# Kernel tuning notes

Measured on AMD Instinct MI355X. Metric: run time of the kernel, lower is better.

Reference implementation:

```python
import jax, jax.numpy as jnp
import numpy as np

B, C, H, W = 4, 128, 256, 256
N, NPOS, KS = 4000, 8, 3
CH = 2 * NPOS  # mask=False -> 2*n_pos offset channels


def setup_inputs() -> dict:
    key = jax.random.key(0)
    ks = jax.random.split(key, 8)
    x = jax.random.normal(ks[0], (B, C, H, W), jnp.float32)
    keypoints = jax.random.uniform(ks[1], (B, N, 2), jnp.float32) * 2.0 - 1.0  # [-1,1]
    w1 = jax.random.normal(ks[2], (CH, C, KS, KS), jnp.float32) * 0.05  # offset conv 3x3
    b1 = jnp.zeros((CH,), jnp.float32)
    w2 = jax.random.normal(ks[3], (CH, CH), jnp.float32) * 0.05        # offset conv 1x1
    b2 = jnp.zeros((CH,), jnp.float32)
    wsf = jax.random.normal(ks[4], (C, C), jnp.float32) * 0.05         # sf_conv 1x1 no bias
    agg_weights = jax.random.uniform(ks[5], (NPOS, C, C), jnp.float32)  # torch.rand init
    return {"x": x, "keypoints": keypoints, "w1": w1, "b1": b1, "w2": w2,
            "b2": b2, "wsf": wsf, "agg_weights": agg_weights}


def _bilinear_sample(img, px, py):
    """grid_sample(mode=bilinear, align_corners=True, padding=zeros) at pixel coords.
    img: (C,H,W); px,py: (M,). Returns (C,M)."""
    c, h, w = img.shape
    x0f = jnp.floor(px); y0f = jnp.floor(py)
    x0 = x0f.astype(jnp.int32); y0 = y0f.astype(jnp.int32)
    wx1 = px - x0f; wx0 = 1.0 - wx1
    wy1 = py - y0f; wy0 = 1.0 - wy1

    def tap(xi, yi, wgt):
        valid = ((xi >= 0) & (xi < w) & (yi >= 0) & (yi < h)).astype(img.dtype)
        v = img[:, jnp.clip(yi, 0, h - 1), jnp.clip(xi, 0, w - 1)]  # (C,M)
        return v * (wgt * valid)

    return (tap(x0, y0, wx0 * wy0) + tap(x0 + 1, y0, wx1 * wy0)
            + tap(x0, y0 + 1, wx0 * wy1) + tap(x0 + 1, y0 + 1, wx1 * wy1))


def _per_image(xi, kpts, w1, b1, w2, b2, wsf, agg_weights):
    wh = jnp.array([W - 1.0, H - 1.0], xi.dtype)
    max_offset = max(H, W) / 4.0
    kwh = (kpts / 2.0 + 0.5) * wh                      # (N,2) pixel coords, >=0
    rc = kwh.astype(jnp.int32)                          # .long() trunc (positive)
    corner = jnp.trunc(rc.astype(jnp.float32) - KS / 2.0 + 1.0).astype(jnp.int32)
    cx = jnp.clip(corner[:, 0], 0, W - 1 - KS)
    cy = jnp.clip(corner[:, 1], 0, H - 1 - KS)
    ar = jnp.arange(KS)
    # patch[n,c,a,b] = xi[c, cy_n+a, cx_n+b]
    patch = xi[:, (cy[:, None] + ar)[:, :, None], (cx[:, None] + ar)[:, None, :]]  # (C,N,KS,KS)
    patch = patch.transpose(1, 0, 2, 3)                 # (N,C,KS,KS)
    # offset network: 3x3 conv (valid) on 3x3 patch == full contraction, then ReLU, 1x1 conv
    h1 = jax.nn.relu(jnp.einsum('nchw,ochw->no', patch, w1) + b1)
    off = jnp.clip(h1 @ w2.T + b2, -max_offset, max_offset)  # (N, 2*NPOS)
    off = off.reshape(-1, 2, NPOS).transpose(0, 2, 1)        # (N,NPOS,2)
    # deform sampling positions; torch normalizes then grid_sample(align_corners=True)
    # maps exactly back to pixel coords, so sample at pixel coords directly
    pos = kwh[:, None, :] + off                              # (N,NPOS,2)
    feats = _bilinear_sample(xi, pos[..., 0].reshape(-1), pos[..., 1].reshape(-1))  # (C,N*NPOS)
    feats = feats.reshape(C, -1, NPOS).transpose(1, 0, 2)    # (N,C,NPOS)
    feats = jax.nn.selu(jnp.einsum('ncp,dc->ndp', feats, wsf))
    descs = jnp.einsum('ncp,pcd->nd', feats, agg_weights)    # (N,C)
    descs = descs / jnp.maximum(jnp.linalg.norm(descs, axis=1, keepdims=True), 1e-12)
    return descs, off


def reference(x, keypoints, w1, b1, w2, b2, wsf, agg_weights):
    f = jax.vmap(lambda xi, k: _per_image(xi, k, w1, b1, w2, b2, wsf, agg_weights))
    descriptors, offsets = f(x, keypoints)
    return descriptors, offsets  # (B,N,C), (B,N,NPOS,2)
```

## Files before the change

### kernel.cpp

```cpp
#include <hip/hip_runtime.h>
#include <math.h>

#define BB 4
#define CC 128
#define HH 256
#define WW 256
#define NN 4000
#define NPOS 8
#define KS 3
#define HWSZ (HH*WW)

#define SELU_ALPHA 1.6732632423543772f
#define SELU_SCALE 1.0507009873554805f
#define MAX_OFFSET 64.0f

typedef unsigned short ushort_t;
typedef short short8 __attribute__((ext_vector_type(8)));
typedef float f32x4 __attribute__((ext_vector_type(4)));
typedef unsigned short ushort4_t __attribute__((ext_vector_type(4)));

#define XT_ELEMS    ((size_t)BB*HH*WW*CC)
#define FEATS_ELEMS ((size_t)BB*NN*NPOS*CC)
#define WSFBF_ELEMS ((size_t)CC*CC)
#define AGGT_ELEMS  ((size_t)NPOS*CC*CC)
#define W1T_ELEMS   ((size_t)16*CC*9)
#define WS_NEEDED   ((XT_ELEMS+FEATS_ELEMS+WSFBF_ELEMS+AGGT_ELEMS+W1T_ELEMS)*sizeof(ushort_t))

__device__ __forceinline__ ushort_t f2bf(float f) {
    unsigned u = __builtin_bit_cast(unsigned, f);
    unsigned r = (u + 0x7FFFu + ((u >> 16) & 1u)) >> 16;
    return (ushort_t)r;
}
__device__ __forceinline__ float bf2f(ushort_t u) {
    return __builtin_bit_cast(float, ((unsigned)u) << 16);
}

__global__ __launch_bounds__(256) void k0p(
    const float* __restrict__ x, ushort_t* __restrict__ xt,
    const float* __restrict__ wsf, const float* __restrict__ agg,
    const float* __restrict__ w1,
    ushort_t* __restrict__ wsf_bf, ushort_t* __restrict__ aggT_bf,
    ushort_t* __restrict__ w1t_bf)
{
    int blk = blockIdx.x;
    const int t = threadIdx.x;
    if (blk >= BB * HH * 4) {
        int i = (blk - BB * HH * 4) * 256 + t;
        if (i < CC * CC) wsf_bf[i] = f2bf(wsf[i]);
        if (i < NPOS * CC * CC) {
            int p = i >> 14, d = (i >> 7) & 127, c = i & 127;
            aggT_bf[i] = f2bf(agg[(p << 14) + (c << 7) + d]);
        }
        if (i < 16 * 1152) {
            int o = i / 1152, e = i - o * 1152, k = e >> 7, c = e & 127;
            w1t_bf[i] = f2bf(w1[o * 1152 + c * 9 + k]);
        }
        return;
    }
    int xc = blk & 3, y = (blk >> 2) & 255, b = blk >> 10;
    int x0 = xc * 64;
    __shared__ ushort_t lds[64][136];

    const float* xb = x + (size_t)b * CC * HWSZ + (size_t)y * WW + x0;
    for (int v = t; v < 2048; v += 256) {
        int c = v >> 4, xo4 = v & 15;
        float4 val = *(const float4*)(xb + (size_t)c * HWSZ + xo4 * 4);
        lds[xo4*4+0][c] = f2bf(val.x);
        lds[xo4*4+1][c] = f2bf(val.y);
        lds[xo4*4+2][c] = f2bf(val.z);
        lds[xo4*4+3][c] = f2bf(val.w);
    }
    __syncthreads();
    ushort_t* outb = xt + ((size_t)b * HWSZ + (size_t)y * WW + x0) * CC;
    for (int v = t; v < 2048; v += 256) {
        int xo = v >> 5, c4 = v & 31;
        ushort4_t val;
        val[0] = lds[xo][c4*4+0];
        val[1] = lds[xo][c4*4+1];
        val[2] = lds[xo][c4*4+2];
        val[3] = lds[xo][c4*4+3];
        *(ushort4_t*)(outb + (size_t)xo * CC + c4 * 4) = val;
    }
}

__global__ __launch_bounds__(256) void k1_mfma(
    const ushort_t* __restrict__ xt, const float* __restrict__ kpts,
    const ushort_t* __restrict__ w1t_bf, const float* __restrict__ b1,
    const float* __restrict__ w2, const float* __restrict__ b2,
    ushort_t* __restrict__ feats_bf, float* __restrict__ out_off)
{
    const int t  = threadIdx.x;
    const int n0 = blockIdx.x * 16;
    const int b  = n0 / NN;
    const ushort_t* xb = xt + (size_t)b * HWSZ * CC;

    __shared__ ushort_t patch[16][1160];
    __shared__ float partials[4][16][16];
    __shared__ float h1f[16][17];
    __shared__ float offs[16][16];
    __shared__ float kw[16][2];
    __shared__ int   cxy[16][2];
    __shared__ int   tapoff[128][4];
    __shared__ float tapw[128][4];

    if (t < 16) {
        float kx = kpts[(size_t)(n0 + t) * 2 + 0];
        float ky = kpts[(size_t)(n0 + t) * 2 + 1];
        float kwx = (kx * 0.5f + 0.5f) * (float)(WW - 1);
        float kwy = (ky * 0.5f + 0.5f) * (float)(HH - 1);
        kw[t][0] = kwx; kw[t][1] = kwy;
        int rcx = (int)kwx, rcy = (int)kwy;
        int cx = (int)truncf((float)rcx - 0.5f);
        int cy = (int)truncf((float)rcy - 0.5f);
        cxy[t][0] = min(max(cx, 0), WW - 1 - KS);
        cxy[t][1] = min(max(cy, 0), HH - 1 - KS);
    }
    __syncthreads();

    #pragma unroll
    for (int it = 0; it < 18; ++it) {
        int v = it * 256 + t;
        int kp = v / 288;
        int rem = v - kp * 288;
        int k = rem >> 5, c4 = rem & 31;
        int kd = k / 3;
        int px = cxy[kp][0] + (k - kd * 3);
        int py = cxy[kp][1] + kd;
        ushort4_t val = *(const ushort4_t*)(xb + ((size_t)(py * WW + px) * CC) + c4 * 4);
        *(ushort4_t*)&patch[kp][k * 128 + c4 * 4] = val;
    }
    __syncthreads();

    {
        int wv = t >> 6, lane = t & 63, m = lane & 15, q = lane >> 4;
        f32x4 hacc = {0.f, 0.f, 0.f, 0.f};
        const ushort_t* arow = &patch[m][wv * 288 + q * 8];
        const ushort_t* brow = w1t_bf + m * 1152 + wv * 288 + q * 8;
        #pragma unroll
        for (int kk = 0; kk < 9; ++kk) {
            short8 a   = *(const short8*)(arow + kk * 32);
            short8 bfr = *(const short8*)(brow + kk * 32);
            hacc = __builtin_amdgcn_mfma_f32_16x16x32_bf16(a, bfr, hacc, 0, 0, 0);
        }
        #pragma unroll
        for (int r = 0; r < 4; ++r) partials[wv][q * 4 + r][m] = hacc[r];
    }
    __syncthreads();
    {
        int kp = t >> 4, o = t & 15;
        float h = partials[0][kp][o] + partials[1][kp][o]
                + partials[2][kp][o] + partials[3][kp][o] + b1[o];
        h1f[kp][o] = fmaxf(h, 0.f);
    }
    __syncthreads();
    {
        int kp = t >> 4, j = t & 15;
        float s = b2[j];
        #pragma unroll
        for (int o = 0; o < 16; ++o) s += h1f[kp][o] * w2[j * 16 + o];
        s = fminf(fmaxf(s, -MAX_OFFSET), MAX_OFFSET);
        offs[kp][j] = s;
        int p = j & 7, comp = j >> 3;
        out_off[((size_t)(n0 + kp) * 8 + p) * 2 + comp] = s;
    }
    __syncthreads();

    if (t < 128) {
        int kp = t >> 3, p = t & 7;
        float px = kw[kp][0] + offs[kp][p];
        float py = kw[kp][1] + offs[kp][8 + p];
        float x0f = floorf(px), y0f = floorf(py);
        int x0 = (int)x0f, y0 = (int)y0f;
        float wx1 = px - x0f, wx0 = 1.f - wx1;
        float wy1 = py - y0f, wy0 = 1.f - wy1;
        int x0c = min(max(x0, 0), WW - 1);
        int x1c = min(max(x0 + 1, 0), WW - 1);
        int y0c = min(max(y0, 0), HH - 1);
        int y1c = min(max(y0 + 1, 0), HH - 1);
        float vx0 = (x0 >= 0 && x0 < WW) ? 1.f : 0.f;
        float vx1 = (x0 + 1 >= 0 && x0 + 1 < WW) ? 1.f : 0.f;
        float vy0 = (y0 >= 0 && y0 < HH) ? 1.f : 0.f;
        float vy1 = (y0 + 1 >= 0 && y0 + 1 < HH) ? 1.f : 0.f;
        tapoff[t][0] = (y0c * WW + x0c) * CC;
        tapoff[t][1] = (y0c * WW + x1c) * CC;
        tapoff[t][2] = (y1c * WW + x0c) * CC;
        tapoff[t][3] = (y1c * WW + x1c) * CC;
        tapw[t][0] = wx0 * wy0 * vx0 * vy0;
        tapw[t][1] = wx1 * wy0 * vx1 * vy0;
        tapw[t][2] = wx0 * wy1 * vx0 * vy1;
        tapw[t][3] = wx1 * wy1 * vx1 * vy1;
    }
    __syncthreads();

    {
        int pair = t >> 1, half = t & 1;
        int kp = pair >> 3, p = pair & 7;
        const ushort_t* s0 = xb + tapoff[pair][0];
        const ushort_t* s1 = xb + tapoff[pair][1];
        const ushort_t* s2 = xb + tapoff[pair][2];
        const ushort_t* s3 = xb + tapoff[pair][3];
        float w00 = tapw[pair][0], w01 = tapw[pair][1];
        float w10 = tapw[pair][2], w11 = tapw[pair][3];
        ushort_t* dst = feats_bf + (size_t)(n0 + kp) * (NPOS * CC) + p * CC + half * 64;
        #pragma unroll
        for (int i = 0; i < 16; ++i) {
            int c = half * 64 + i * 4;
            ushort4_t t0 = *(const ushort4_t*)(s0 + c);
            ushort4_t t1 = *(const ushort4_t*)(s1 + c);
            ushort4_t t2 = *(const ushort4_t*)(s2 + c);
            ushort4_t t3 = *(const ushort4_t*)(s3 + c);
            ushort4_t r;
            #pragma unroll
            for (int j = 0; j < 4; ++j) {
                float v = bf2f(t0[j]) * w00 + bf2f(t1[j]) * w01
                        + bf2f(t2[j]) * w10 + bf2f(t3[j]) * w11;
                r[j] = f2bf(v);
            }
            *(ushort4_t*)(dst + i * 4) = r;
        }
    }
}

__global__ __launch_bounds__(256) void k34_mfma(
    const ushort_t* __restrict__ feats_bf, const ushort_t* __restrict__ wsf_bf,
    const ushort_t* __restrict__ aggT_bf, float* __restrict__ out_desc)
{
    const int t    = threadIdx.x;
    const int wv   = t >> 6;
    const int lane = t & 63;
    const int m    = lane & 15;
    const int q    = lane >> 4;
    const int n0   = blockIdx.x * 16;
    const int R0   = n0 * NPOS;

    __shared__ float g[CC * CC];
    __shared__ float dbuf[16 * 132];
    __shared__ float rn[16];

    for (int rti = 0; rti < 2; ++rti) {
        int rt = wv * 2 + rti;
        short8 afr[4];
        const ushort_t* arow = feats_bf + (size_t)(R0 + rt * 16 + m) * CC + q * 8;
        #pragma unroll
        for (int kk = 0; kk < 4; ++kk)
            afr[kk] = *(const short8*)(arow + kk * 32);
        for (int ct = 0; ct < 8; ++ct) {
            const ushort_t* brow = wsf_bf + (ct * 16 + m) * CC + q * 8;
            f32x4 acc = {0.f, 0.f, 0.f, 0.f};
            #pragma unroll
            for (int kk = 0; kk < 4; ++kk) {
                short8 bfr = *(const short8*)(brow + kk * 32);
                acc = __builtin_amdgcn_mfma_f32_16x16x32_bf16(afr[kk], bfr, acc, 0, 0, 0);
            }
            #pragma unroll
            for (int r = 0; r < 4; ++r) {
                float s = acc[r];
                s = (s > 0.f) ? (SELU_SCALE * s)
                              : (SELU_SCALE * SELU_ALPHA * (expf(s) - 1.f));
                int row = rt * 16 + q * 4 + r;
                int col = ct * 16 + m;
                unsigned byte = ((unsigned)(row * CC + col) << 2) ^ ((unsigned)((row >> 3) & 7) << 4);
                *(float*)((char*)g + byte) = s;
            }
        }
    }
    __syncthreads();

    f32x4 acc2[2];
    acc2[0] = (f32x4){0.f, 0.f, 0.f, 0.f};
    acc2[1] = (f32x4){0.f, 0.f, 0.f, 0.f};
    const int ctbase = wv * 2;
    const unsigned swz = (unsigned)(m & 7) << 4;
    for (int kk = 0; kk < 32; ++kk) {
        int p  = kk >> 2;
        int c0 = (kk & 3) * 32 + q * 8;
        int rowA = m * 8 + p;
        unsigned lin = (unsigned)(rowA * CC + c0) << 2;
        f32x4 v0 = *(const f32x4*)((const char*)g + (lin ^ swz));
        f32x4 v1 = *(const f32x4*)((const char*)g + ((lin + 16u) ^ swz));
        short8 afr;
        #pragma unroll
        for (int j = 0; j < 4; ++j) afr[j] = (short)f2bf(v0[j]);
        #pragma unroll
        for (int j = 0; j < 4; ++j) afr[4 + j] = (short)f2bf(v1[j]);
        #pragma unroll
        for (int i = 0; i < 2; ++i) {
            int ct = ctbase + i;
            const ushort_t* brow = aggT_bf + (size_t)(p * CC + ct * 16 + m) * CC + (kk & 3) * 32 + q * 8;
            short8 bfr = *(const short8*)brow;
            acc2[i] = __builtin_amdgcn_mfma_f32_16x16x32_bf16(afr, bfr, acc2[i], 0, 0, 0);
        }
    }
    #pragma unroll
    for (int i = 0; i < 2; ++i) {
        int ct = ctbase + i;
        #pragma unroll
        for (int r = 0; r < 4; ++r) {
            int n = q * 4 + r;
            dbuf[n * 132 + ct * 16 + m] = acc2[i][r];
        }
    }
    __syncthreads();

    {
        int n = t >> 4, l = t & 15;
        float s = 0.f;
        #pragma unroll
        for (int j = 0; j < 8; ++j) { float v = dbuf[n * 132 + l + j * 16]; s += v * v; }
        s += __shfl_xor(s, 1);
        s += __shfl_xor(s, 2);
        s += __shfl_xor(s, 4);
        s += __shfl_xor(s, 8);
        if (l == 0) rn[n] = 1.0f / fmaxf(sqrtf(s), 1e-12f);
    }
    __syncthreads();
    for (int idx = t; idx < 2048; idx += 256) {
        int n = idx >> 7, d = idx & 127;
        out_desc[(size_t)(n0 + n) * CC + d] = dbuf[n * 132 + d] * rn[n];
    }
}

__global__ __launch_bounds__(256, 4) void sddh_baseline(
    const float* __restrict__ x, const float* __restrict__ keypoints,
    const float* __restrict__ w1, const float* __restrict__ b1,
    const float* __restrict__ w2, const float* __restrict__ b2,
    const float* __restrict__ wsf, const float* __restrict__ agg,
    float* __restrict__ out_desc, float* __restrict__ out_off)
{
    const int bn = blockIdx.x;
    const int b  = bn / NN;
    const int t  = threadIdx.x;
    const float* xi = x + (size_t)b * CC * HWSZ;

    __shared__ float patch[CC * 9];
    __shared__ float conv_part[16][17];
    __shared__ float h1s[16];
    __shared__ float offs[16];
    __shared__ float feats[CC][NPOS];
    __shared__ float cpart2[CC][NPOS];
    __shared__ float g[CC][NPOS];
    __shared__ float dpart[CC];
    __shared__ float desc[CC];
    __shared__ float sq[128];
    __shared__ float kxy[2];

    if (t == 0) {
        float kx = keypoints[(size_t)bn * 2 + 0];
        float ky = keypoints[(size_t)bn * 2 + 1];
        kxy[0] = (kx * 0.5f + 0.5f) * (float)(WW - 1);
        kxy[1] = (ky * 0.5f + 0.5f) * (float)(HH - 1);
    }
    __syncthreads();
    const float kwx = kxy[0], kwy = kxy[1];
    const int rcx = (int)kwx, rcy = (int)kwy;
    int cx = (int)truncf((float)rcx - 0.5f);
    int cy = (int)truncf((float)rcy - 0.5f);
    cx = min(max(cx, 0), WW - 1 - KS);
    cy = min(max(cy, 0), HH - 1 - KS);

    for (int e = t; e < CC * 9; e += 256) {
        int c = e / 9, k = e % 9;
        int dy = k / 3, dx = k % 3;
        patch[e] = xi[(size_t)c * HWSZ + (cy + dy) * WW + (cx + dx)];
    }
    __syncthreads();
    {
        int o = t & 15, j = t >> 4;
        float acc = 0.f;
        const float* wo = w1 + o * (CC * 9);
        for (int e = j; e < CC * 9; e += 16) acc += patch[e] * wo[e];
        conv_part[o][j] = acc;
    }
    __syncthreads();
    if (t < 16) {
        float s = b1[t];
        #pragma unroll
        for (int j = 0; j < 16; j++) s += conv_part[t][j];
        h1s[t] = fmaxf(s, 0.f);
    }
    __syncthreads();
    if (t < 16) {
        float s = b2[t];
        #pragma unroll
        for (int k = 0; k < 16; k++) s += h1s[k] * w2[t * 16 + k];
        s = fminf(fmaxf(s, -MAX_OFFSET), MAX_OFFSET);
        offs[t] = s;
        int idx = (t < 8) ? (bn * 16 + t * 2) : (bn * 16 + (t - 8) * 2 + 1);
        out_off[idx] = s;
    }
    __syncthreads();

    for (int e = t; e < CC * NPOS; e += 256) {
        int c = e & 127, p = e >> 7;
        float px = kwx + offs[p];
        float py = kwy + offs[8 + p];
        float x0f = floorf(px), y0f = floorf(py);
        int x0 = (int)x0f, y0 = (int)y0f;
        float wx1 = px - x0f, wx0 = 1.f - wx1;
        float wy1 = py - y0f, wy0 = 1.f - wy1;
        const float* xc = xi + (size_t)c * HWSZ;
        int x0c = min(max(x0, 0), WW - 1);
        int x1c = min(max(x0 + 1, 0), WW - 1);
        int y0c = min(max(y0, 0), HH - 1);
        int y1c = min(max(y0 + 1, 0), HH - 1);
        float vx0 = (x0 >= 0 && x0 < WW) ? 1.f : 0.f;
        float vx1 = (x0 + 1 >= 0 && x0 + 1 < WW) ? 1.f : 0.f;
        float vy0 = (y0 >= 0 && y0 < HH) ? 1.f : 0.f;
        float vy1 = (y0 + 1 >= 0 && y0 + 1 < HH) ? 1.f : 0.f;
        float v = 0.f;
        v += xc[y0c * WW + x0c] * (wx0 * wy0) * (vx0 * vy0);
        v += xc[y0c * WW + x1c] * (wx1 * wy0) * (vx1 * vy0);
        v += xc[y1c * WW + x0c] * (wx0 * wy1) * (vx0 * vy1);
        v += xc[y1c * WW + x1c] * (wx1 * wy1) * (vx1 * vy1);
        feats[c][p] = v;
    }
    __syncthreads();
    {
        int d = t & 127, chalf = t >> 7;
        float acc[NPOS];
        #pragma unroll
        for (int p = 0; p < NPOS; p++) acc[p] = 0.f;
        const float* wrow = wsf + d * CC;
        int c0 = chalf * 64;
        for (int c = c0; c < c0 + 64; c++) {
            float wv = wrow[c];
            #pragma unroll
            for (int p = 0; p < NPOS; p++) acc[p] += feats[c][p] * wv;
        }
        if (chalf) {
            #pragma unroll
            for (int p = 0; p < NPOS; p++) cpart2[d][p] = acc[p];
        }
        __syncthreads();
        if (!chalf) {
            #pragma unroll
            for (int p = 0; p < NPOS; p++) {
                float s = acc[p] + cpart2[d][p];
                s = (s > 0.f) ? (SELU_SCALE * s)
                              : (SELU_SCALE * SELU_ALPHA * (expf(s) - 1.f));
                g[d][p] = s;
            }
        }
    }
    __syncthreads();
    {
        int d = t & 127, half = t >> 7;
        float acc = 0.f;
        int p0 = half * 4;
        for (int p = p0; p < p0 + 4; p++) {
            const float* ap = agg + (size_t)p * CC * CC;
            for (int e = 0; e < CC; e++) acc += g[e][p] * ap[e * CC + d];
        }
        if (half) dpart[d] = acc;
        __syncthreads();
        if (!half) {
            float v = acc + dpart[d];
            desc[d] = v;
            sq[d] = v * v;
        }
    }
    __syncthreads();
    if (t < 64) sq[t] += sq[t + 64]; __syncthreads();
    if (t < 32) sq[t] += sq[t + 32]; __syncthreads();
    if (t < 16) sq[t] += sq[t + 16]; __syncthreads();
    if (t < 8)  sq[t] += sq[t + 8];  __syncthreads();
    if (t < 4)  sq[t] += sq[t + 4];  __syncthreads();
    if (t < 2)  sq[t] += sq[t + 2];  __syncthreads();
    if (t == 0) sq[0] = fmaxf(sqrtf(sq[0] + sq[1]), 1e-12f);
    __syncthreads();
    if (t < 128) out_desc[(size_t)bn * CC + t] = desc[t] / sq[0];
}

extern "C" void kernel_launch(void* const* d_in, const int* in_sizes, int n_in,
                              void* d_out, int out_size, void* d_ws, size_t ws_size,
                              hipStream_t stream) {
    const float* x    = (const float*)d_in[0];
    const float* kpts = (const float*)d_in[1];
    const float* w1   = (const float*)d_in[2];
    const float* b1   = (const float*)d_in[3];
    const float* w2   = (const float*)d_in[4];
    const float* b2   = (const float*)d_in[5];
    const float* wsf  = (const float*)d_in[6];
    const float* agg  = (const float*)d_in[7];

    float* out_desc = (float*)d_out;
    float* out_off  = (float*)d_out + (size_t)BB * NN * CC;

    if (ws_size < WS_NEEDED) {
        hipLaunchKernelGGL(sddh_baseline, dim3(BB * NN), dim3(256), 0, stream,
                           x, kpts, w1, b1, w2, b2, wsf, agg, out_desc, out_off);
        return;
    }

    ushort_t* xt       = (ushort_t*)d_ws;
    ushort_t* feats_bf = xt + XT_ELEMS;
    ushort_t* wsf_bf   = feats_bf + FEATS_ELEMS;
    ushort_t* aggT_bf  = wsf_bf + WSFBF_ELEMS;
    ushort_t* w1t_bf   = aggT_bf + AGGT_ELEMS;

    hipLaunchKernelGGL(k0p, dim3(BB * HH * 4 + 512), dim3(256), 0, stream,
                       x, xt, wsf, agg, w1, wsf_bf, aggT_bf, w1t_bf);
    hipLaunchKernelGGL(k1_mfma, dim3(BB * NN / 16), dim3(256), 0, stream,
                       xt, kpts, w1t_bf, b1, w2, b2, feats_bf, out_off);
    hipLaunchKernelGGL(k34_mfma, dim3(BB * NN / 16), dim3(256), 0, stream,
                       feats_bf, wsf_bf, aggT_bf, out_desc);
}
```

Measured before the change: 121.9 us.

## Fuse offset/sampling kernel with descriptor GEMM kernel, keep feats in LDS

Merges the offset-prediction and bilinear-sampling kernel with the wsf/agg MFMA kernel, so sampled features stay in swizzled LDS instead of making a round trip through a global bf16 buffer. The 3x3 patch for the offset conv is read straight from global into MFMA operands rather than staged in LDS. The SELU intermediate is now stored in LDS as bf16 instead of fp32, which halves its footprint and drops the per-use conversion. In exchange it saves one kernel launch and the global feats traffic, but raises LDS per block to about 64KB, which limits occupancy (launch bounds now ask for 2 blocks).

```diff
diff --git a/kernel.cpp b/kernel.cpp
--- a/kernel.cpp
+++ b/kernel.cpp
@@ -20,11 +20,10 @@
 typedef unsigned short ushort4_t __attribute__((ext_vector_type(4)));
 
 #define XT_ELEMS    ((size_t)BB*HH*WW*CC)
-#define FEATS_ELEMS ((size_t)BB*NN*NPOS*CC)
 #define WSFBF_ELEMS ((size_t)CC*CC)
 #define AGGT_ELEMS  ((size_t)NPOS*CC*CC)
 #define W1T_ELEMS   ((size_t)16*CC*9)
-#define WS_NEEDED   ((XT_ELEMS+FEATS_ELEMS+WSFBF_ELEMS+AGGT_ELEMS+W1T_ELEMS)*sizeof(ushort_t))
+#define WS_NEEDED   ((XT_ELEMS+WSFBF_ELEMS+AGGT_ELEMS+W1T_ELEMS)*sizeof(ushort_t))
 
 __device__ __forceinline__ ushort_t f2bf(float f) {
     unsigned u = __builtin_bit_cast(unsigned, f);
@@ -83,25 +82,37 @@
     }
 }
 
-__global__ __launch_bounds__(256) void k1_mfma(
+__global__ __launch_bounds__(256, 2) void k14_fused(
     const ushort_t* __restrict__ xt, const float* __restrict__ kpts,
     const ushort_t* __restrict__ w1t_bf, const float* __restrict__ b1,
     const float* __restrict__ w2, const float* __restrict__ b2,
-    ushort_t* __restrict__ feats_bf, float* __restrict__ out_off)
+    const ushort_t* __restrict__ wsf_bf, const ushort_t* __restrict__ aggT_bf,
+    float* __restrict__ out_desc, float* __restrict__ out_off)
 {
-    const int t  = threadIdx.x;
-    const int n0 = blockIdx.x * 16;
-    const int b  = n0 / NN;
+    const int t    = threadIdx.x;
+    const int wv   = t >> 6;
+    const int lane = t & 63;
+    const int m    = lane & 15;
+    const int q    = lane >> 4;
+    const int n0   = blockIdx.x * 16;
+    const int b    = n0 / NN;
     const ushort_t* xb = xt + (size_t)b * HWSZ * CC;
 
-    __shared__ ushort_t patch[16][1160];
-    __shared__ float partials[4][16][16];
-    __shared__ float h1f[16][17];
-    __shared__ float offs[16][16];
+    __shared__ ushort_t feats[CC * CC];
+    __shared__ ushort_t g[CC * CC];
+    __shared__ union {
+        struct {
+            float partials[4][16][16];
+            float h1f[16][17];
+            float offs[16][16];
+            int   tapoff[128][4];
+            float tapw[128][4];
+        } a;
+        float dbuf[16 * 132];
+    } u;
     __shared__ float kw[16][2];
     __shared__ int   cxy[16][2];
-    __shared__ int   tapoff[128][4];
-    __shared__ float tapw[128][4];
+    __shared__ float rn[16];
 
     if (t < 16) {
         float kx = kpts[(size_t)(n0 + t) * 2 + 0];
@@ -117,49 +128,38 @@
     }
     __syncthreads();
 
-    #pragma unroll
-    for (int it = 0; it < 18; ++it) {
-        int v = it * 256 + t;
-        int kp = v / 288;
-        int rem = v - kp * 288;
-        int k = rem >> 5, c4 = rem & 31;
-        int kd = k / 3;
-        int px = cxy[kp][0] + (k - kd * 3);
-        int py = cxy[kp][1] + kd;
-        ushort4_t val = *(const ushort4_t*)(xb + ((size_t)(py * WW + px) * CC) + c4 * 4);
-        *(ushort4_t*)&patch[kp][k * 128 + c4 * 4] = val;
-    }
-    __syncthreads();
-
-    {
-        int wv = t >> 6, lane = t & 63, m = lane & 15, q = lane >> 4;
+    {
+        int px0 = cxy[m][0], py0 = cxy[m][1];
         f32x4 hacc = {0.f, 0.f, 0.f, 0.f};
-        const ushort_t* arow = &patch[m][wv * 288 + q * 8];
         const ushort_t* brow = w1t_bf + m * 1152 + wv * 288 + q * 8;
         #pragma unroll
         for (int kk = 0; kk < 9; ++kk) {
-            short8 a   = *(const short8*)(arow + kk * 32);
+            int e = wv * 288 + kk * 32 + q * 8;
+            int k = e >> 7, c = e & 127;
+            int kd = k / 3, kx2 = k - kd * 3;
+            const ushort_t* src = xb + ((size_t)((py0 + kd) * WW + px0 + kx2)) * CC + c;
+            short8 a   = *(const short8*)src;
             short8 bfr = *(const short8*)(brow + kk * 32);
             hacc = __builtin_amdgcn_mfma_f32_16x16x32_bf16(a, bfr, hacc, 0, 0, 0);
         }
         #pragma unroll
-        for (int r = 0; r < 4; ++r) partials[wv][q * 4 + r][m] = hacc[r];
+        for (int r = 0; r < 4; ++r) u.a.partials[wv][q * 4 + r][m] = hacc[r];
     }
     __syncthreads();
     {
         int kp = t >> 4, o = t & 15;
-        float h = partials[0][kp][o] + partials[1][kp][o]
-                + partials[2][kp][o] + partials[3][kp][o] + b1[o];
-        h1f[kp][o] = fmaxf(h, 0.f);
+        float h = u.a.partials[0][kp][o] + u.a.partials[1][kp][o]
+                + u.a.partials[2][kp][o] + u.a.partials[3][kp][o] + b1[o];
+        u.a.h1f[kp][o] = fmaxf(h, 0.f);
     }
     __syncthreads();
     {
         int kp = t >> 4, j = t & 15;
         float s = b2[j];
         #pragma unroll
-        for (int o = 0; o < 16; ++o) s += h1f[kp][o] * w2[j * 16 + o];
+        for (int o = 0; o < 16; ++o) s += u.a.h1f[kp][o] * w2[j * 16 + o];
         s = fminf(fmaxf(s, -MAX_OFFSET), MAX_OFFSET);
-        offs[kp][j] = s;
+        u.a.offs[kp][j] = s;
         int p = j & 7, comp = j >> 3;
         out_off[((size_t)(n0 + kp) * 8 + p) * 2 + comp] = s;
     }
@@ -167,8 +167,8 @@
 
     if (t < 128) {
         int kp = t >> 3, p = t & 7;
-        float px = kw[kp][0] + offs[kp][p];
-        float py = kw[kp][1] + offs[kp][8 + p];
+        float px = kw[kp][0] + u.a.offs[kp][p];
+        float py = kw[kp][1] + u.a.offs[kp][8 + p];
         float x0f = floorf(px), y0f = floorf(py);
         int x0 = (int)x0f, y0 = (int)y0f;
         float wx1 = px - x0f, wx0 = 1.f - wx1;
@@ -181,27 +181,27 @@
         float vx1 = (x0 + 1 >= 0 && x0 + 1 < WW) ? 1.f : 0.f;
         float vy0 = (y0 >= 0 && y0 < HH) ? 1.f : 0.f;
         float vy1 = (y0 + 1 >= 0 && y0 + 1 < HH) ? 1.f : 0.f;
-        tapoff[t][0] = (y0c * WW + x0c) * CC;
-        tapoff[t][1] = (y0c * WW + x1c) * CC;
-        tapoff[t][2] = (y1c * WW + x0c) * CC;
-        tapoff[t][3] = (y1c * WW + x1c) * CC;
-        tapw[t][0] = wx0 * wy0 * vx0 * vy0;
-        tapw[t][1] = wx1 * wy0 * vx1 * vy0;
-        tapw[t][2] = wx0 * wy1 * vx0 * vy1;
-        tapw[t][3] = wx1 * wy1 * vx1 * vy1;
+        u.a.tapoff[t][0] = (y0c * WW + x0c) * CC;
+        u.a.tapoff[t][1] = (y0c * WW + x1c) * CC;
+        u.a.tapoff[t][2] = (y1c * WW + x0c) * CC;
+        u.a.tapoff[t][3] = (y1c * WW + x1c) * CC;
+        u.a.tapw[t][0] = wx0 * wy0 * vx0 * vy0;
+        u.a.tapw[t][1] = wx1 * wy0 * vx1 * vy0;
+        u.a.tapw[t][2] = wx0 * wy1 * vx0 * vy1;
+        u.a.tapw[t][3] = wx1 * wy1 * vx1 * vy1;
     }
     __syncthreads();
 
     {
         int pair = t >> 1, half = t & 1;
-        int kp = pair >> 3, p = pair & 7;
-        const ushort_t* s0 = xb + tapoff[pair][0];
-        const ushort_t* s1 = xb + tapoff[pair][1];
-        const ushort_t* s2 = xb + tapoff[pair][2];
-        const ushort_t* s3 = xb + tapoff[pair][3];
-        float w00 = tapw[pair][0], w01 = tapw[pair][1];
-        float w10 = tapw[pair][2], w11 = tapw[pair][3];
-        ushort_t* dst = feats_bf + (size_t)(n0 + kp) * (NPOS * CC) + p * CC + half * 64;
+        const ushort_t* s0 = xb + u.a.tapoff[pair][0];
+        const ushort_t* s1 = xb + u.a.tapoff[pair][1];
+        const ushort_t* s2 = xb + u.a.tapoff[pair][2];
+        const ushort_t* s3 = xb + u.a.tapoff[pair][3];
+        float w00 = u.a.tapw[pair][0], w01 = u.a.tapw[pair][1];
+        float w10 = u.a.tapw[pair][2], w11 = u.a.tapw[pair][3];
+        unsigned rbase = (unsigned)(pair * 256);
+        unsigned key   = ((unsigned)(pair & 7)) << 4;
         #pragma unroll
         for (int i = 0; i < 16; ++i) {
             int c = half * 64 + i * 4;
@@ -209,41 +209,29 @@
             ushort4_t t1 = *(const ushort4_t*)(s1 + c);
             ushort4_t t2 = *(const ushort4_t*)(s2 + c);
             ushort4_t t3 = *(const ushort4_t*)(s3 + c);
-            ushort4_t r;
+            ushort4_t r4;
             #pragma unroll
             for (int j = 0; j < 4; ++j) {
                 float v = bf2f(t0[j]) * w00 + bf2f(t1[j]) * w01
                         + bf2f(t2[j]) * w10 + bf2f(t3[j]) * w11;
-                r[j] = f2bf(v);
+                r4[j] = f2bf(v);
             }
-            *(ushort4_t*)(dst + i * 4) = r;
-        }
-    }
-}
-
-__global__ __launch_bounds__(256) void k34_mfma(
-    const ushort_t* __restrict__ feats_bf, const ushort_t* __restrict__ wsf_bf,
-    const ushort_t* __restrict__ aggT_bf, float* __restrict__ out_desc)
-{
-    const int t    = threadIdx.x;
-    const int wv   = t >> 6;
-    const int lane = t & 63;
-    const int m    = lane & 15;
-    const int q    = lane >> 4;
-    const int n0   = blockIdx.x * 16;
-    const int R0   = n0 * NPOS;
-
-    __shared__ float g[CC * CC];
-    __shared__ float dbuf[16 * 132];
-    __shared__ float rn[16];
+            unsigned byte = (rbase + (unsigned)c * 2) ^ key;
+            *(ushort4_t*)((char*)feats + byte) = r4;
+        }
+    }
+    __syncthreads();
 
     for (int rti = 0; rti < 2; ++rti) {
         int rt = wv * 2 + rti;
+        int r  = rt * 16 + m;
+        unsigned key = ((unsigned)(r & 7)) << 4;
         short8 afr[4];
-        const ushort_t* arow = feats_bf + (size_t)(R0 + rt * 16 + m) * CC + q * 8;
-        #pragma unroll
-        for (int kk = 0; kk < 4; ++kk)
-            afr[kk] = *(const short8*)(arow + kk * 32);
+        #pragma unroll
+        for (int kk = 0; kk < 4; ++kk) {
+            unsigned byte = ((unsigned)(r * 256 + q * 16 + kk * 64)) ^ key;
+            afr[kk] = *(const short8*)((const char*)feats + byte);
+        }
         for (int ct = 0; ct < 8; ++ct) {
             const ushort_t* brow = wsf_bf + (ct * 16 + m) * CC + q * 8;
             f32x4 acc = {0.f, 0.f, 0.f, 0.f};
@@ -253,14 +241,15 @@
                 acc = __builtin_amdgcn_mfma_f32_16x16x32_bf16(afr[kk], bfr, acc, 0, 0, 0);
             }
             #pragma unroll
-            for (int r = 0; r < 4; ++r) {
-                float s = acc[r];
+            for (int rr = 0; rr < 4; ++rr) {
+                float s = acc[rr];
                 s = (s > 0.f) ? (SELU_SCALE * s)
                               : (SELU_SCALE * SELU_ALPHA * (expf(s) - 1.f));
-                int row = rt * 16 + q * 4 + r;
+                int row = rt * 16 + q * 4 + rr;
                 int col = ct * 16 + m;
-                unsigned byte = ((unsigned)(row * CC + col) << 2) ^ ((unsigned)((row >> 3) & 7) << 4);
-                *(float*)((char*)g + byte) = s;
+                unsigned byte = ((unsigned)(row * 256 + col * 2))
+                              ^ (((unsigned)((row >> 3) & 7)) << 4);
+                *(ushort_t*)((char*)g + byte) = f2bf(s);
             }
         }
     }
@@ -270,23 +259,17 @@
     acc2[0] = (f32x4){0.f, 0.f, 0.f, 0.f};
     acc2[1] = (f32x4){0.f, 0.f, 0.f, 0.f};
     const int ctbase = wv * 2;
-    const unsigned swz = (unsigned)(m & 7) << 4;
     for (int kk = 0; kk < 32; ++kk) {
-        int p  = kk >> 2;
-        int c0 = (kk & 3) * 32 + q * 8;
+        int p    = kk >> 2;
         int rowA = m * 8 + p;
-        unsigned lin = (unsigned)(rowA * CC + c0) << 2;
-        f32x4 v0 = *(const f32x4*)((const char*)g + (lin ^ swz));
-        f32x4 v1 = *(const f32x4*)((const char*)g + ((lin + 16u) ^ swz));
-        short8 afr;
-        #pragma unroll
-        for (int j = 0; j < 4; ++j) afr[j] = (short)f2bf(v0[j]);
-        #pragma unroll
-        for (int j = 0; j < 4; ++j) afr[4 + j] = (short)f2bf(v1[j]);
+        unsigned byte = ((unsigned)(rowA * 256 + (kk & 3) * 64 + q * 16))
+                      ^ (((unsigned)((rowA >> 3) & 7)) << 4);
+        short8 afr = *(const short8*)((const char*)g + byte);
         #pragma unroll
         for (int i = 0; i < 2; ++i) {
             int ct = ctbase + i;
-            const ushort_t* brow = aggT_bf + (size_t)(p * CC + ct * 16 + m) * CC + (kk & 3) * 32 + q * 8;
+            const ushort_t* brow = aggT_bf + (size_t)(p * CC + ct * 16 + m) * CC
+                                 + (kk & 3) * 32 + q * 8;
             short8 bfr = *(const short8*)brow;
             acc2[i] = __builtin_amdgcn_mfma_f32_16x16x32_bf16(afr, bfr, acc2[i], 0, 0, 0);
         }
@@ -295,9 +278,9 @@
     for (int i = 0; i < 2; ++i) {
         int ct = ctbase + i;
         #pragma unroll
-        for (int r = 0; r < 4; ++r) {
-            int n = q * 4 + r;
-            dbuf[n * 132 + ct * 16 + m] = acc2[i][r];
+        for (int rr = 0; rr < 4; ++rr) {
+            int n = q * 4 + rr;
+            u.dbuf[n * 132 + ct * 16 + m] = acc2[i][rr];
         }
     }
     __syncthreads();
@@ -306,7 +289,7 @@
         int n = t >> 4, l = t & 15;
         float s = 0.f;
         #pragma unroll
-        for (int j = 0; j < 8; ++j) { float v = dbuf[n * 132 + l + j * 16]; s += v * v; }
+        for (int j = 0; j < 8; ++j) { float v = u.dbuf[n * 132 + l + j * 16]; s += v * v; }
         s += __shfl_xor(s, 1);
         s += __shfl_xor(s, 2);
         s += __shfl_xor(s, 4);
@@ -316,7 +299,7 @@
     __syncthreads();
     for (int idx = t; idx < 2048; idx += 256) {
         int n = idx >> 7, d = idx & 127;
-        out_desc[(size_t)(n0 + n) * CC + d] = dbuf[n * 132 + d] * rn[n];
+        out_desc[(size_t)(n0 + n) * CC + d] = u.dbuf[n * 132 + d] * rn[n];
     }
 }
 
@@ -492,16 +475,14 @@
         return;
     }
 
-    ushort_t* xt       = (ushort_t*)d_ws;
-    ushort_t* feats_bf = xt + XT_ELEMS;
-    ushort_t* wsf_bf   = feats_bf + FEATS_ELEMS;
-    ushort_t* aggT_bf  = wsf_bf + WSFBF_ELEMS;
-    ushort_t* w1t_bf   = aggT_bf + AGGT_ELEMS;
+    ushort_t* xt      = (ushort_t*)d_ws;
+    ushort_t* wsf_bf  = xt + XT_ELEMS;
+    ushort_t* aggT_bf = wsf_bf + WSFBF_ELEMS;
+    ushort_t* w1t_bf  = aggT_bf + AGGT_ELEMS;
 
     hipLaunchKernelGGL(k0p, dim3(BB * HH * 4 + 512), dim3(256), 0, stream,
                        x, xt, wsf, agg, w1, wsf_bf, aggT_bf, w1t_bf);
-    hipLaunchKernelGGL(k1_mfma, dim3(BB * NN / 16), dim3(256), 0, stream,
-                       xt, kpts, w1t_bf, b1, w2, b2, feats_bf, out_off);
-    hipLaunchKernelGGL(k34_mfma, dim3(BB * NN / 16), dim3(256), 0, stream,
-                       feats_bf, wsf_bf, aggT_bf, out_desc);
-}
+    hipLaunchKernelGGL(k14_fused, dim3(BB * NN / 16), dim3(256), 0, stream,
+                       xt, kpts, w1t_bf, b1, w2, b2, wsf_bf, aggT_bf,
+                       out_desc, out_off);
+}
```

Result: faster. 106.8 us (-12.4%).
